# Kernel optimization log

Hardware: AMD Instinct MI355X
Metric: run time of the kernel (lower is better)

Reference implementation:

```python
import jax, jax.numpy as jnp
import numpy as np

DIM_EMB = 512
NB_HEADS = 16
NB_LAYERS = 3
BSZ = 256
NB_NODES = 500
NEG_INF = -1e9


def my_mha(q, K, V, nb_heads, mask=None, clip_value=None):
    # q: (bsz, 1, d); K, V: (bsz, n, d); mask: (bsz, n) bool (True = masked)
    bsz, n, d = K.shape
    dh = d // nb_heads
    qh = q.reshape(bsz, nb_heads, dh)            # split emb into heads
    Kh = K.reshape(bsz, n, nb_heads, dh)
    Vh = V.reshape(bsz, n, nb_heads, dh)
    scores = jnp.einsum('bhd,bnhd->bhn', qh, Kh) / jnp.sqrt(jnp.asarray(dh, q.dtype))
    if clip_value is not None:
        scores = clip_value * jnp.tanh(scores)
    if mask is not None:
        scores = jnp.where(mask[:, None, :], jnp.asarray(NEG_INF, scores.dtype), scores)
    w = jax.nn.softmax(scores, axis=-1)          # (bsz, H, n)
    out = jnp.einsum('bhn,bnhd->bhd', w, Vh).reshape(bsz, 1, d)
    attn_weights = w.mean(axis=1)[:, None, :]    # (bsz, 1, n)
    return out, attn_weights


def setup_inputs() -> dict:
    key = jax.random.key(0)
    ks = jax.random.split(key, 5)
    s = 1.0 / np.sqrt(DIM_EMB)
    return {
        'query': jax.random.normal(ks[0], (BSZ, 1, DIM_EMB), jnp.float32),
        'K_att': jax.random.normal(ks[1], (BSZ, NB_NODES, DIM_EMB * NB_LAYERS), jnp.float32),
        'V_att': jax.random.normal(ks[2], (BSZ, NB_NODES, DIM_EMB * NB_LAYERS), jnp.float32),
        'mask': jnp.zeros((BSZ, NB_NODES), jnp.bool_),
        'W0_w': jax.random.normal(ks[3], (DIM_EMB, DIM_EMB), jnp.float32) * s,
        'W0_b': jnp.zeros((DIM_EMB,), jnp.float32),
        'Wqf_w': jax.random.normal(ks[4], (DIM_EMB, DIM_EMB), jnp.float32) * s,
        'Wqf_b': jnp.zeros((DIM_EMB,), jnp.float32),
    }


def reference(query, K_att, V_att, mask, W0_w, W0_b, Wqf_w, Wqf_b):
    d = DIM_EMB
    attn_weights = None
    for l in range(NB_LAYERS):
        K_l = K_att[:, :, l * d:(l + 1) * d]
        V_l = V_att[:, :, l * d:(l + 1) * d]
        if l < NB_LAYERS - 1:
            out, _ = my_mha(query, K_l, V_l, NB_HEADS, mask)
            query = out @ W0_w.T + W0_b
        else:
            q_final = (query @ Wqf_w.T + Wqf_b).reshape(-1, 1, d)
            _, attn_weights = my_mha(q_final, K_l, V_l, 1, mask, clip_value=10.0)
    return attn_weights[:, 0, :]  # (bsz, nb_nodes)
```

## Files before the change

kernel.cpp:

```cpp
#include <hip/hip_runtime.h>
#include <cstdint>
#include <cstddef>

#define BSZ 256
#define NN 500
#define D 512
#define H 16
#define KSTRIDE 1536
#define NEG_INF -1000000000.0f

#define WS_Q1    0
#define WS_QF    131072
#define WS_WT0   262144
#define WS_WCT   524288
#define WS_BC    786432

__global__ __launch_bounds__(256) void prep(
    const float* __restrict__ W0, const float* __restrict__ Wqf,
    const float* __restrict__ b0, const float* __restrict__ bqf,
    float* __restrict__ Wt0, float* __restrict__ Wct, float* __restrict__ bc)
{
    __shared__ float As[32][33];
    __shared__ float Bs[32][33];

    const int t  = threadIdx.x;
    const int bx = blockIdx.x, by = blockIdx.y;

    if (blockIdx.z == 0) {
        const int tx = t & 31, ty = t >> 5;
        const int c0 = bx * 32, r0 = by * 32;
#pragma unroll
        for (int i = 0; i < 32; i += 8)
            As[ty + i][tx] = W0[(size_t)(r0 + ty + i) * D + c0 + tx];
        __syncthreads();
#pragma unroll
        for (int i = 0; i < 32; i += 8)
            Wt0[(size_t)(c0 + ty + i) * D + r0 + tx] = As[tx][ty + i];
        return;
    }

    const int j0 = by * 32;
    const int d0 = bx * 32;
    const int lr  = t >> 3;
    const int lc4 = (t & 7) * 4;
    const int ty2 = (t >> 4) * 2;
    const int tx2 = (t & 15) * 2;

    float c00 = 0.f, c01 = 0.f, c10 = 0.f, c11 = 0.f;

    for (int k0 = 0; k0 < D; k0 += 32) {
        const float4 av = *reinterpret_cast<const float4*>(
            Wqf + (size_t)(j0 + lr) * D + k0 + lc4);
        const float4 bv = *reinterpret_cast<const float4*>(
            W0 + (size_t)(k0 + lr) * D + d0 + lc4);
        As[lr][lc4] = av.x; As[lr][lc4 + 1] = av.y;
        As[lr][lc4 + 2] = av.z; As[lr][lc4 + 3] = av.w;
        Bs[lr][lc4] = bv.x; Bs[lr][lc4 + 1] = bv.y;
        Bs[lr][lc4 + 2] = bv.z; Bs[lr][lc4 + 3] = bv.w;
        __syncthreads();
#pragma unroll 8
        for (int kk = 0; kk < 32; ++kk) {
            const float a0 = As[ty2][kk], a1 = As[ty2 + 1][kk];
            const float v0 = Bs[kk][tx2], v1 = Bs[kk][tx2 + 1];
            c00 += a0 * v0; c01 += a0 * v1;
            c10 += a1 * v0; c11 += a1 * v1;
        }
        __syncthreads();
    }

    As[tx2][ty2]         = c00;
    As[tx2 + 1][ty2]     = c01;
    As[tx2][ty2 + 1]     = c10;
    As[tx2 + 1][ty2 + 1] = c11;
    __syncthreads();
#pragma unroll
    for (int i = 0; i < 4; ++i)
        Wct[(size_t)(d0 + lr) * D + j0 + lc4 + i] = As[lr][lc4 + i];

    if (bx == 0 && t < 32) {
        const int j = j0 + t;
        float s = 0.f;
        for (int k = 0; k < D; ++k)
            s += Wqf[(size_t)j * D + k] * b0[k];
        bc[j] = s + bqf[j];
    }
}

__global__ __launch_bounds__(1024) void attn_layer_fused(
    const float* __restrict__ q_in,
    const float* __restrict__ Katt,
    const float* __restrict__ Vatt,
    const unsigned char* __restrict__ mask,
    const float* __restrict__ Wt,
    const float* __restrict__ bias,
    float* __restrict__ q_out,
    int loff)
{
    __shared__ __align__(16) float part_acc[16 * D];
    __shared__ float part_m[16 * H];
    __shared__ float part_l[16 * H];
    __shared__ __align__(16) float out_lds[D];
    __shared__ float gemv_part[2 * D];

    const int b = blockIdx.x;
    const int t = threadIdx.x;
    const int r = t & 63;
    const int g = t >> 6;

    const float* qp = q_in + (size_t)b * D + r * 8;
    const float4 qa = *reinterpret_cast<const float4*>(qp);
    const float4 qb = *reinterpret_cast<const float4*>(qp + 4);

    const float* Kb = Katt + (size_t)b * NN * KSTRIDE + loff;
    const float* Vb = Vatt + (size_t)b * NN * KSTRIDE + loff;
    const unsigned char* mb = mask + (size_t)b * NN;

    float m = -3.4e38f, lsum = 0.f;
    float4 acc0 = {0.f, 0.f, 0.f, 0.f};
    float4 acc1 = {0.f, 0.f, 0.f, 0.f};

#pragma unroll 2
    for (int n = g; n < NN; n += 16) {
        const float* kr = Kb + (size_t)n * KSTRIDE + r * 8;
        const float* vr = Vb + (size_t)n * KSTRIDE + r * 8;
        const float4 ka  = *reinterpret_cast<const float4*>(kr);
        const float4 kb4 = *reinterpret_cast<const float4*>(kr + 4);
        const float4 va  = *reinterpret_cast<const float4*>(vr);
        const float4 vb4 = *reinterpret_cast<const float4*>(vr + 4);

        float s = qa.x * ka.x + qa.y * ka.y + qa.z * ka.z + qa.w * ka.w
                + qb.x * kb4.x + qb.y * kb4.y + qb.z * kb4.z + qb.w * kb4.w;
        s += __shfl_xor(s, 1);
        s += __shfl_xor(s, 2);
        float sc = s * 0.17677669529663687f;
        if (mb[n]) sc = NEG_INF;

        const float mn   = fmaxf(m, sc);
        const float corr = __expf(m - mn);
        const float e    = __expf(sc - mn);
        lsum = lsum * corr + e;
        acc0.x = acc0.x * corr + e * va.x;
        acc0.y = acc0.y * corr + e * va.y;
        acc0.z = acc0.z * corr + e * va.z;
        acc0.w = acc0.w * corr + e * va.w;
        acc1.x = acc1.x * corr + e * vb4.x;
        acc1.y = acc1.y * corr + e * vb4.y;
        acc1.z = acc1.z * corr + e * vb4.z;
        acc1.w = acc1.w * corr + e * vb4.w;
        m = mn;
    }

    *reinterpret_cast<float4*>(part_acc + g * D + r * 8)     = acc0;
    *reinterpret_cast<float4*>(part_acc + g * D + r * 8 + 4) = acc1;
    if ((r & 3) == 0) {
        part_m[g * H + (r >> 2)] = m;
        part_l[g * H + (r >> 2)] = lsum;
    }
    __syncthreads();

    if (t < D) {
        const int hd = t >> 5;
        float ms = -3.4e38f;
#pragma unroll
        for (int g2 = 0; g2 < 16; ++g2)
            ms = fmaxf(ms, part_m[g2 * H + hd]);
        float ls = 0.f, o = 0.f;
#pragma unroll
        for (int g2 = 0; g2 < 16; ++g2) {
            const float w = __expf(part_m[g2 * H + hd] - ms);
            ls += part_l[g2 * H + hd] * w;
            o  += part_acc[g2 * D + t] * w;
        }
        out_lds[t] = o / ls;
    }
    __syncthreads();

    {
        const int j = t & 511;
        const int half = t >> 9;
        const float* Wp = Wt + (size_t)half * 256 * D + j;
        const float* a  = out_lds + half * 256;
        float acc = 0.f;
#pragma unroll 4
        for (int k = 0; k < 256; ++k)
            acc += a[k] * Wp[(size_t)k * D];
        gemv_part[half * D + j] = acc;
    }
    __syncthreads();
    if (t < D)
        q_out[(size_t)b * D + t] = gemv_part[t] + gemv_part[D + t] + bias[t];
}

__global__ __launch_bounds__(1024) void final_layer(
    const float* __restrict__ qf,
    const float* __restrict__ Katt,
    const unsigned char* __restrict__ mask,
    float* __restrict__ out)
{
    __shared__ __align__(16) float qf_lds[D];
    __shared__ float s_lds[NN];
    __shared__ float red[16];
    __shared__ float bm, bs;

    const int b = blockIdx.x;
    const int t = threadIdx.x;

    if (t < D) qf_lds[t] = qf[(size_t)b * D + t];
    __syncthreads();

    const int wv   = t >> 6;
    const int l    = t & 63;
    const int half = l >> 5;
    const int l32  = l & 31;

    const float* qpp = qf_lds + l32 * 16;
    const float4 q0 = *reinterpret_cast<const float4*>(qpp);
    const float4 q1 = *reinterpret_cast<const float4*>(qpp + 4);
    const float4 q2 = *reinterpret_cast<const float4*>(qpp + 8);
    const float4 q3 = *reinterpret_cast<const float4*>(qpp + 12);

    const float* Kb = Katt + (size_t)b * NN * KSTRIDE + 1024;
    const unsigned char* mb = mask + (size_t)b * NN;

    for (int n = wv * 2 + half; n < NN; n += 32) {
        const float* kr = Kb + (size_t)n * KSTRIDE + l32 * 16;
        const float4 k0 = *reinterpret_cast<const float4*>(kr);
        const float4 k1 = *reinterpret_cast<const float4*>(kr + 4);
        const float4 k2 = *reinterpret_cast<const float4*>(kr + 8);
        const float4 k3 = *reinterpret_cast<const float4*>(kr + 12);
        float s = q0.x * k0.x + q0.y * k0.y + q0.z * k0.z + q0.w * k0.w
                + q1.x * k1.x + q1.y * k1.y + q1.z * k1.z + q1.w * k1.w
                + q2.x * k2.x + q2.y * k2.y + q2.z * k2.z + q2.w * k2.w
                + q3.x * k3.x + q3.y * k3.y + q3.z * k3.z + q3.w * k3.w;
#pragma unroll
        for (int o = 1; o < 32; o <<= 1) s += __shfl_xor(s, o);
        if (l32 == 0) {
            float sc = 10.0f * tanhf(s * 0.044194173824159216f);
            if (mb[n]) sc = NEG_INF;
            s_lds[n] = sc;
        }
    }
    __syncthreads();

    const float v = (t < NN) ? s_lds[t] : -3.4e38f;
    float m = v;
#pragma unroll
    for (int o = 1; o < 64; o <<= 1) m = fmaxf(m, __shfl_xor(m, o));
    if (l == 0) red[wv] = m;
    __syncthreads();
    if (t == 0) {
        float mm = red[0];
#pragma unroll
        for (int i = 1; i < 16; ++i) mm = fmaxf(mm, red[i]);
        bm = mm;
    }
    __syncthreads();
    const float e = (t < NN) ? __expf(v - bm) : 0.f;
    float ssum = e;
#pragma unroll
    for (int o = 1; o < 64; o <<= 1) ssum += __shfl_xor(ssum, o);
    if (l == 0) red[wv] = ssum;
    __syncthreads();
    if (t == 0) {
        float s2 = 0.f;
#pragma unroll
        for (int i = 0; i < 16; ++i) s2 += red[i];
        bs = 1.0f / s2;
    }
    __syncthreads();
    if (t < NN) out[(size_t)b * NN + t] = e * bs;
}

extern "C" void kernel_launch(void* const* d_in, const int* in_sizes, int n_in,
                              void* d_out, int out_size, void* d_ws, size_t ws_size,
                              hipStream_t stream) {
    const float* query = (const float*)d_in[0];
    const float* Katt  = (const float*)d_in[1];
    const float* Vatt  = (const float*)d_in[2];
    const unsigned char* mask = (const unsigned char*)d_in[3];
    const float* W0w = (const float*)d_in[4];
    const float* W0b = (const float*)d_in[5];
    const float* Wfw = (const float*)d_in[6];
    const float* Wfb = (const float*)d_in[7];

    float* out = (float*)d_out;
    float* ws  = (float*)d_ws;
    float* q1  = ws + WS_Q1;
    float* qf  = ws + WS_QF;
    float* Wt0 = ws + WS_WT0;
    float* Wct = ws + WS_WCT;
    float* bc  = ws + WS_BC;

    prep<<<dim3(16, 16, 2), 256, 0, stream>>>(W0w, Wfw, W0b, Wfb, Wt0, Wct, bc);

    attn_layer_fused<<<BSZ, 1024, 0, stream>>>(query, Katt, Vatt, mask,
                                               Wt0, W0b, q1, 0);
    attn_layer_fused<<<BSZ, 1024, 0, stream>>>(q1, Katt, Vatt, mask,
                                               Wct, bc, qf, 512);
    final_layer<<<BSZ, 1024, 0, stream>>>(qf, Katt, mask, out);
}
```

Before: 310.6 us.

## Fuse all three attention layers into a single per-batch kernel

Replaces the two per-layer attention launches and the final-layer launch with one kernel in which each block processes its batch row through all layers. The intermediate queries stay in shared memory instead of going through global workspace. The mask is staged in shared memory once. Each thread now keeps two independent online-softmax streams over alternating node rows, which adds memory-level parallelism at the cost of extra registers and a merge step.

New measurement: 309.0 us. No clear change (-0.5%).

```diff
diff --git a/kernel.cpp b/kernel.cpp
--- a/kernel.cpp
+++ b/kernel.cpp
@@ -9,11 +9,9 @@
 #define KSTRIDE 1536
 #define NEG_INF -1000000000.0f
 
-#define WS_Q1    0
-#define WS_QF    131072
-#define WS_WT0   262144
-#define WS_WCT   524288
-#define WS_BC    786432
+#define WS_WT0   0
+#define WS_WCT   262144
+#define WS_BC    524288
 
 __global__ __launch_bounds__(256) void prep(
     const float* __restrict__ W0, const float* __restrict__ Wqf,
@@ -86,189 +84,236 @@
     }
 }
 
-__global__ __launch_bounds__(1024) void attn_layer_fused(
-    const float* __restrict__ q_in,
+__device__ __forceinline__ float4 ld4(const float* p) {
+    return *reinterpret_cast<const float4*>(p);
+}
+
+__device__ __forceinline__ float head_score(const float4 qa, const float4 qb,
+                                            const float4 k0, const float4 k1)
+{
+    float s = qa.x * k0.x + qa.y * k0.y + qa.z * k0.z + qa.w * k0.w
+            + qb.x * k1.x + qb.y * k1.y + qb.z * k1.z + qb.w * k1.w;
+    s += __shfl_xor(s, 1);
+    s += __shfl_xor(s, 2);
+    return s * 0.17677669529663687f;
+}
+
+__device__ __forceinline__ void online_upd(float& m, float& l, float4& a0, float4& a1,
+                                           const float sc, const float4 v0, const float4 v1)
+{
+    const float mn   = fmaxf(m, sc);
+    const float corr = __expf(m - mn);
+    const float e    = __expf(sc - mn);
+    l = l * corr + e;
+    a0.x = a0.x * corr + e * v0.x;
+    a0.y = a0.y * corr + e * v0.y;
+    a0.z = a0.z * corr + e * v0.z;
+    a0.w = a0.w * corr + e * v0.w;
+    a1.x = a1.x * corr + e * v1.x;
+    a1.y = a1.y * corr + e * v1.y;
+    a1.z = a1.z * corr + e * v1.z;
+    a1.w = a1.w * corr + e * v1.w;
+    m = mn;
+}
+
+__device__ __forceinline__ void stream_attn(
+    const float4 qa, const float4 qb,
+    const float* __restrict__ Kb, const float* __restrict__ Vb,
+    const unsigned char* __restrict__ mask_lds,
+    const int g, const int r,
+    float* __restrict__ part_acc, float* __restrict__ part_m,
+    float* __restrict__ part_l)
+{
+    float mA = -3.4e38f, lA = 0.f;
+    float4 aA0 = {0.f,0.f,0.f,0.f}, aA1 = {0.f,0.f,0.f,0.f};
+    float mB = -3.4e38f, lB = 0.f;
+    float4 aB0 = {0.f,0.f,0.f,0.f}, aB1 = {0.f,0.f,0.f,0.f};
+
+    for (int n = g; n < NN; n += 32) {
+        const int n2 = n + 16;
+        const float* krA = Kb + (size_t)n * KSTRIDE + r * 8;
+        const float* vrA = Vb + (size_t)n * KSTRIDE + r * 8;
+        const float4 kA0 = ld4(krA), kA1 = ld4(krA + 4);
+        const float4 vA0 = ld4(vrA), vA1 = ld4(vrA + 4);
+
+        if (n2 < NN) {
+            const float* krB = Kb + (size_t)n2 * KSTRIDE + r * 8;
+            const float* vrB = Vb + (size_t)n2 * KSTRIDE + r * 8;
+            const float4 kB0 = ld4(krB), kB1 = ld4(krB + 4);
+            const float4 vB0 = ld4(vrB), vB1 = ld4(vrB + 4);
+
+            float scA = head_score(qa, qb, kA0, kA1);
+            if (mask_lds[n]) scA = NEG_INF;
+            online_upd(mA, lA, aA0, aA1, scA, vA0, vA1);
+
+            float scB = head_score(qa, qb, kB0, kB1);
+            if (mask_lds[n2]) scB = NEG_INF;
+            online_upd(mB, lB, aB0, aB1, scB, vB0, vB1);
+        } else {
+            float scA = head_score(qa, qb, kA0, kA1);
+            if (mask_lds[n]) scA = NEG_INF;
+            online_upd(mA, lA, aA0, aA1, scA, vA0, vA1);
+        }
+    }
+
+    const float mn = fmaxf(mA, mB);
+    const float wA = __expf(mA - mn), wB = __expf(mB - mn);
+    const float lm = lA * wA + lB * wB;
+    float4 o0, o1;
+    o0.x = aA0.x * wA + aB0.x * wB;  o0.y = aA0.y * wA + aB0.y * wB;
+    o0.z = aA0.z * wA + aB0.z * wB;  o0.w = aA0.w * wA + aB0.w * wB;
+    o1.x = aA1.x * wA + aB1.x * wB;  o1.y = aA1.y * wA + aB1.y * wB;
+    o1.z = aA1.z * wA + aB1.z * wB;  o1.w = aA1.w * wA + aB1.w * wB;
+
+    *reinterpret_cast<float4*>(part_acc + g * D + r * 8)     = o0;
+    *reinterpret_cast<float4*>(part_acc + g * D + r * 8 + 4) = o1;
+    if ((r & 3) == 0) {
+        part_m[g * H + (r >> 2)] = mn;
+        part_l[g * H + (r >> 2)] = lm;
+    }
+}
+
+__global__ __launch_bounds__(1024) void fused_all(
+    const float* __restrict__ query,
     const float* __restrict__ Katt,
     const float* __restrict__ Vatt,
     const unsigned char* __restrict__ mask,
-    const float* __restrict__ Wt,
-    const float* __restrict__ bias,
-    float* __restrict__ q_out,
-    int loff)
+    const float* __restrict__ Wt0, const float* __restrict__ b0,
+    const float* __restrict__ Wct, const float* __restrict__ bc,
+    float* __restrict__ out)
 {
     __shared__ __align__(16) float part_acc[16 * D];
     __shared__ float part_m[16 * H];
     __shared__ float part_l[16 * H];
     __shared__ __align__(16) float out_lds[D];
+    __shared__ __align__(16) float q_lds[D];
     __shared__ float gemv_part[2 * D];
+    __shared__ unsigned char mask_lds[512];
+    __shared__ float s_lds[NN];
+    __shared__ float red[16];
+    __shared__ float bm, bs;
 
     const int b = blockIdx.x;
     const int t = threadIdx.x;
     const int r = t & 63;
     const int g = t >> 6;
 
-    const float* qp = q_in + (size_t)b * D + r * 8;
-    const float4 qa = *reinterpret_cast<const float4*>(qp);
-    const float4 qb = *reinterpret_cast<const float4*>(qp + 4);
-
-    const float* Kb = Katt + (size_t)b * NN * KSTRIDE + loff;
-    const float* Vb = Vatt + (size_t)b * NN * KSTRIDE + loff;
-    const unsigned char* mb = mask + (size_t)b * NN;
-
-    float m = -3.4e38f, lsum = 0.f;
-    float4 acc0 = {0.f, 0.f, 0.f, 0.f};
-    float4 acc1 = {0.f, 0.f, 0.f, 0.f};
-
-#pragma unroll 2
-    for (int n = g; n < NN; n += 16) {
-        const float* kr = Kb + (size_t)n * KSTRIDE + r * 8;
-        const float* vr = Vb + (size_t)n * KSTRIDE + r * 8;
-        const float4 ka  = *reinterpret_cast<const float4*>(kr);
-        const float4 kb4 = *reinterpret_cast<const float4*>(kr + 4);
-        const float4 va  = *reinterpret_cast<const float4*>(vr);
-        const float4 vb4 = *reinterpret_cast<const float4*>(vr + 4);
-
-        float s = qa.x * ka.x + qa.y * ka.y + qa.z * ka.z + qa.w * ka.w
-                + qb.x * kb4.x + qb.y * kb4.y + qb.z * kb4.z + qb.w * kb4.w;
-        s += __shfl_xor(s, 1);
-        s += __shfl_xor(s, 2);
-        float sc = s * 0.17677669529663687f;
-        if (mb[n]) sc = NEG_INF;
-
-        const float mn   = fmaxf(m, sc);
-        const float corr = __expf(m - mn);
-        const float e    = __expf(sc - mn);
-        lsum = lsum * corr + e;
-        acc0.x = acc0.x * corr + e * va.x;
-        acc0.y = acc0.y * corr + e * va.y;
-        acc0.z = acc0.z * corr + e * va.z;
-        acc0.w = acc0.w * corr + e * va.w;
-        acc1.x = acc1.x * corr + e * vb4.x;
-        acc1.y = acc1.y * corr + e * vb4.y;
-        acc1.z = acc1.z * corr + e * vb4.z;
-        acc1.w = acc1.w * corr + e * vb4.w;
-        m = mn;
-    }
-
-    *reinterpret_cast<float4*>(part_acc + g * D + r * 8)     = acc0;
-    *reinterpret_cast<float4*>(part_acc + g * D + r * 8 + 4) = acc1;
-    if ((r & 3) == 0) {
-        part_m[g * H + (r >> 2)] = m;
-        part_l[g * H + (r >> 2)] = lsum;
-    }
+    if (t < 512) mask_lds[t] = (t < NN) ? mask[(size_t)b * NN + t] : 0;
+
+    const float* Kbase = Katt + (size_t)b * NN * KSTRIDE;
+    const float* Vbase = Vatt + (size_t)b * NN * KSTRIDE;
+
+    float4 qa = ld4(query + (size_t)b * D + r * 8);
+    float4 qb = ld4(query + (size_t)b * D + r * 8 + 4);
     __syncthreads();
 
-    if (t < D) {
-        const int hd = t >> 5;
-        float ms = -3.4e38f;
-#pragma unroll
-        for (int g2 = 0; g2 < 16; ++g2)
-            ms = fmaxf(ms, part_m[g2 * H + hd]);
-        float ls = 0.f, o = 0.f;
-#pragma unroll
-        for (int g2 = 0; g2 < 16; ++g2) {
-            const float w = __expf(part_m[g2 * H + hd] - ms);
-            ls += part_l[g2 * H + hd] * w;
-            o  += part_acc[g2 * D + t] * w;
-        }
-        out_lds[t] = o / ls;
-    }
-    __syncthreads();
+#pragma unroll 1
+    for (int layer = 0; layer < 2; ++layer) {
+        const int loff = layer * 512;
+        stream_attn(qa, qb, Kbase + loff, Vbase + loff, mask_lds, g, r,
+                    part_acc, part_m, part_l);
+        __syncthreads();
+
+        if (t < D) {
+            const int hd = t >> 5;
+            float ms = -3.4e38f;
+#pragma unroll
+            for (int g2 = 0; g2 < 16; ++g2)
+                ms = fmaxf(ms, part_m[g2 * H + hd]);
+            float ls = 0.f, o = 0.f;
+#pragma unroll
+            for (int g2 = 0; g2 < 16; ++g2) {
+                const float w = __expf(part_m[g2 * H + hd] - ms);
+                ls += part_l[g2 * H + hd] * w;
+                o  += part_acc[g2 * D + t] * w;
+            }
+            out_lds[t] = o / ls;
+        }
+        __syncthreads();
+
+        {
+            const float* Wt   = layer ? Wct : Wt0;
+            const float* bias = layer ? bc  : b0;
+            const int j = t & 511;
+            const int half = t >> 9;
+            const float* Wp = Wt + (size_t)half * 256 * D + j;
+            const float* a  = out_lds + half * 256;
+            float acc = 0.f;
+#pragma unroll 4
+            for (int k = 0; k < 256; ++k)
+                acc += a[k] * Wp[(size_t)k * D];
+            gemv_part[half * D + j] = acc;
+            __syncthreads();
+            if (t < D) q_lds[t] = gemv_part[t] + gemv_part[D + t] + bias[t];
+            __syncthreads();
+        }
+
+        qa = ld4(q_lds + r * 8);
+        qb = ld4(q_lds + r * 8 + 4);
+    }
 
     {
-        const int j = t & 511;
-        const int half = t >> 9;
-        const float* Wp = Wt + (size_t)half * 256 * D + j;
-        const float* a  = out_lds + half * 256;
-        float acc = 0.f;
-#pragma unroll 4
-        for (int k = 0; k < 256; ++k)
-            acc += a[k] * Wp[(size_t)k * D];
-        gemv_part[half * D + j] = acc;
-    }
-    __syncthreads();
-    if (t < D)
-        q_out[(size_t)b * D + t] = gemv_part[t] + gemv_part[D + t] + bias[t];
-}
-
-__global__ __launch_bounds__(1024) void final_layer(
-    const float* __restrict__ qf,
-    const float* __restrict__ Katt,
-    const unsigned char* __restrict__ mask,
-    float* __restrict__ out)
-{
-    __shared__ __align__(16) float qf_lds[D];
-    __shared__ float s_lds[NN];
-    __shared__ float red[16];
-    __shared__ float bm, bs;
-
-    const int b = blockIdx.x;
-    const int t = threadIdx.x;
-
-    if (t < D) qf_lds[t] = qf[(size_t)b * D + t];
-    __syncthreads();
-
-    const int wv   = t >> 6;
-    const int l    = t & 63;
-    const int half = l >> 5;
-    const int l32  = l & 31;
-
-    const float* qpp = qf_lds + l32 * 16;
-    const float4 q0 = *reinterpret_cast<const float4*>(qpp);
-    const float4 q1 = *reinterpret_cast<const float4*>(qpp + 4);
-    const float4 q2 = *reinterpret_cast<const float4*>(qpp + 8);
-    const float4 q3 = *reinterpret_cast<const float4*>(qpp + 12);
-
-    const float* Kb = Katt + (size_t)b * NN * KSTRIDE + 1024;
-    const unsigned char* mb = mask + (size_t)b * NN;
-
-    for (int n = wv * 2 + half; n < NN; n += 32) {
-        const float* kr = Kb + (size_t)n * KSTRIDE + l32 * 16;
-        const float4 k0 = *reinterpret_cast<const float4*>(kr);
-        const float4 k1 = *reinterpret_cast<const float4*>(kr + 4);
-        const float4 k2 = *reinterpret_cast<const float4*>(kr + 8);
-        const float4 k3 = *reinterpret_cast<const float4*>(kr + 12);
-        float s = q0.x * k0.x + q0.y * k0.y + q0.z * k0.z + q0.w * k0.w
-                + q1.x * k1.x + q1.y * k1.y + q1.z * k1.z + q1.w * k1.w
-                + q2.x * k2.x + q2.y * k2.y + q2.z * k2.z + q2.w * k2.w
-                + q3.x * k3.x + q3.y * k3.y + q3.z * k3.z + q3.w * k3.w;
-#pragma unroll
-        for (int o = 1; o < 32; o <<= 1) s += __shfl_xor(s, o);
-        if (l32 == 0) {
-            float sc = 10.0f * tanhf(s * 0.044194173824159216f);
-            if (mb[n]) sc = NEG_INF;
-            s_lds[n] = sc;
-        }
-    }
-    __syncthreads();
-
-    const float v = (t < NN) ? s_lds[t] : -3.4e38f;
-    float m = v;
-#pragma unroll
-    for (int o = 1; o < 64; o <<= 1) m = fmaxf(m, __shfl_xor(m, o));
-    if (l == 0) red[wv] = m;
-    __syncthreads();
-    if (t == 0) {
-        float mm = red[0];
-#pragma unroll
-        for (int i = 1; i < 16; ++i) mm = fmaxf(mm, red[i]);
-        bm = mm;
-    }
-    __syncthreads();
-    const float e = (t < NN) ? __expf(v - bm) : 0.f;
-    float ssum = e;
-#pragma unroll
-    for (int o = 1; o < 64; o <<= 1) ssum += __shfl_xor(ssum, o);
-    if (l == 0) red[wv] = ssum;
-    __syncthreads();
-    if (t == 0) {
-        float s2 = 0.f;
-#pragma unroll
-        for (int i = 0; i < 16; ++i) s2 += red[i];
-        bs = 1.0f / s2;
-    }
-    __syncthreads();
-    if (t < NN) out[(size_t)b * NN + t] = e * bs;
+        const int wv   = t >> 6;
+        const int l    = t & 63;
+        const int half = l >> 5;
+        const int l32  = l & 31;
+
+        const float* qpp = q_lds + l32 * 16;
+        const float4 f0 = ld4(qpp);
+        const float4 f1 = ld4(qpp + 4);
+        const float4 f2 = ld4(qpp + 8);
+        const float4 f3 = ld4(qpp + 12);
+
+        const float* Kb2 = Kbase + 1024;
+
+        for (int n = wv * 2 + half; n < NN; n += 32) {
+            const float* kr = Kb2 + (size_t)n * KSTRIDE + l32 * 16;
+            const float4 k0 = ld4(kr);
+            const float4 k1 = ld4(kr + 4);
+            const float4 k2 = ld4(kr + 8);
+            const float4 k3 = ld4(kr + 12);
+            float s = f0.x * k0.x + f0.y * k0.y + f0.z * k0.z + f0.w * k0.w
+                    + f1.x * k1.x + f1.y * k1.y + f1.z * k1.z + f1.w * k1.w
+                    + f2.x * k2.x + f2.y * k2.y + f2.z * k2.z + f2.w * k2.w
+                    + f3.x * k3.x + f3.y * k3.y + f3.z * k3.z + f3.w * k3.w;
+#pragma unroll
+            for (int o = 1; o < 32; o <<= 1) s += __shfl_xor(s, o);
+            if (l32 == 0) {
+                float sc = 10.0f * tanhf(s * 0.044194173824159216f);
+                if (mask_lds[n]) sc = NEG_INF;
+                s_lds[n] = sc;
+            }
+        }
+        __syncthreads();
+
+        const float v = (t < NN) ? s_lds[t] : -3.4e38f;
+        float m = v;
+#pragma unroll
+        for (int o = 1; o < 64; o <<= 1) m = fmaxf(m, __shfl_xor(m, o));
+        if (l == 0) red[wv] = m;
+        __syncthreads();
+        if (t == 0) {
+            float mm = red[0];
+#pragma unroll
+            for (int i = 1; i < 16; ++i) mm = fmaxf(mm, red[i]);
+            bm = mm;
+        }
+        __syncthreads();
+        const float e = (t < NN) ? __expf(v - bm) : 0.f;
+        float ssum = e;
+#pragma unroll
+        for (int o = 1; o < 64; o <<= 1) ssum += __shfl_xor(ssum, o);
+        if (l == 0) red[wv] = ssum;
+        __syncthreads();
+        if (t == 0) {
+            float s2 = 0.f;
+#pragma unroll
+            for (int i = 0; i < 16; ++i) s2 += red[i];
+            bs = 1.0f / s2;
+        }
+        __syncthreads();
+        if (t < NN) out[(size_t)b * NN + t] = e * bs;
+    }
 }
 
 extern "C" void kernel_launch(void* const* d_in, const int* in_sizes, int n_in,
@@ -285,17 +330,11 @@
 
     float* out = (float*)d_out;
     float* ws  = (float*)d_ws;
-    float* q1  = ws + WS_Q1;
-    float* qf  = ws + WS_QF;
     float* Wt0 = ws + WS_WT0;
     float* Wct = ws + WS_WCT;
     float* bc  = ws + WS_BC;
 
     prep<<<dim3(16, 16, 2), 256, 0, stream>>>(W0w, Wfw, W0b, Wfb, Wt0, Wct, bc);
-
-    attn_layer_fused<<<BSZ, 1024, 0, stream>>>(query, Katt, Vatt, mask,
-                                               Wt0, W0b, q1, 0);
-    attn_layer_fused<<<BSZ, 1024, 0, stream>>>(q1, Katt, Vatt, mask,
-                                               Wct, bc, qf, 512);
-    final_layer<<<BSZ, 1024, 0, stream>>>(qf, Katt, mask, out);
-}
+    fused_all<<<BSZ, 1024, 0, stream>>>(query, Katt, Vatt, mask,
+                                        Wt0, W0b, Wct, bc, out);
+}
```
